# Optimization experiments

Hardware: AMD Instinct MI355X
Metric: run time of the kernel (lower is better)

## Reference

```python
import jax, jax.numpy as jnp
import numpy as np

HC = 4
C = 256
TMAX = 20
RMS_EPS = 1e-6
PRE_EPS = 0.0
SINKHORN_EPS = 1e-6
POST_MULT = 2.0


def setup_inputs() -> dict:
    key = jax.random.key(0)
    k1, k2, k3 = jax.random.split(key, 3)
    B, S = 8, 4096
    m = HC * HC + 2 * HC
    x = jax.random.normal(k1, (B, S, HC, C), dtype=jnp.float32)
    phi = jax.random.normal(k2, (HC * C, m), dtype=jnp.float32) * 0.02
    b = jnp.zeros((m,), dtype=jnp.float32)
    W = jax.random.normal(k3, (C, C), dtype=jnp.float32) * (1.0 / np.sqrt(C))
    return {
        "x": x, "phi": phi, "b": b,
        "alpha_pre": jnp.float32(1.0), "alpha_post": jnp.float32(1.0), "alpha_res": jnp.float32(1.0),
        "W": W,
    }


def _mhc_coeffs(x, phi, b, alpha_pre, alpha_post, alpha_res):
    # x: [..., HC, C] -> flatten streams, project, RMS-normalize logits.
    lead = x.shape[:-2]
    v = x.reshape(lead + (HC * C,))
    logits = jnp.einsum('...k,km->...m', v, phi)            # [..., m]
    rms = jnp.sqrt(jnp.mean(logits * logits, axis=-1, keepdims=True) + RMS_EPS)
    y = logits / rms + b                                     # [..., m]
    pre = y[..., :HC]
    post = y[..., HC:2 * HC]
    res = y[..., 2 * HC:].reshape(lead + (HC, HC))
    h_pre = jax.nn.sigmoid(alpha_pre * pre) + PRE_EPS        # [..., HC]
    h_post = POST_MULT * jax.nn.sigmoid(alpha_post * post)   # [..., HC]
    # Sinkhorn-Knopp: make exp(alpha_res * res) approximately doubly stochastic.
    P = jnp.exp(alpha_res * res)                             # [..., HC, HC]

    def step(P, _):
        P = P / (jnp.sum(P, axis=-1, keepdims=True) + SINKHORN_EPS)  # row norm
        P = P / (jnp.sum(P, axis=-2, keepdims=True) + SINKHORN_EPS)  # col norm
        return P, None

    P, _ = jax.lax.scan(step, P, None, length=TMAX)
    return h_pre, h_post, P


def reference(x, phi, b, alpha_pre, alpha_post, alpha_res, W):
    h_pre, h_post, h_res = _mhc_coeffs(x, phi, b, alpha_pre, alpha_post, alpha_res)
    # Pre-aggregate streams: x_in = sum_i h_pre[i] * x[i]
    x_in = jnp.einsum('...i,...ic->...c', h_pre, x)          # [..., C]
    # Wrapped layer: nn.Linear(C, C, bias=False) -> x_in @ W.T
    f_out = x_in @ W.T                                       # [..., C]
    # Post + residual: x_out[o] = sum_i h_res[o,i]*x[i] + h_post[o]*f_out
    x_out = jnp.einsum('...oi,...ic->...oc', h_res, x) + h_post[..., :, None] * f_out[..., None, :]
    return x_out
```

## Files before the change

### kernel.cpp

```cpp
#include <hip/hip_runtime.h>

typedef __attribute__((ext_vector_type(4))) float floatx4;
typedef __attribute__((ext_vector_type(8))) short short8;

__device__ __forceinline__ unsigned short f2bf(float f) {
    union { float f; unsigned int i; } v; v.f = f;
    unsigned int x = v.i;
    unsigned int r = (x + 0x7FFFu + ((x >> 16) & 1u)) >> 16;
    return (unsigned short)r;
}

__device__ __forceinline__ unsigned int cvtpk_bf16(float lo, float hi) {
    unsigned int r;
    asm("v_cvt_pk_bf16_f32 %0, %1, %2" : "=v"(r) : "v"(lo), "v"(hi));
    return r;
}

template<int CTRL>
__device__ __forceinline__ float dppf(float x) {
    return __int_as_float(__builtin_amdgcn_update_dpp(
        0, __float_as_int(x), CTRL, 0xF, 0xF, false));
}

__global__ void mhc_prep(const float* __restrict__ phi, const float* __restrict__ W,
                         unsigned short* __restrict__ phiF, unsigned short* __restrict__ WF) {
    int e = blockIdx.x * 256 + threadIdx.x;
    if (e < 32768) {
        int j = e & 7, lane = (e >> 3) & 63, nt = (e >> 9) & 1, ks = e >> 10;
        int n = nt * 16 + (lane & 15);
        int k = ks * 32 + ((lane >> 4) & 3) * 8 + j;
        float v = (n < 24) ? phi[k * 24 + n] : 0.0f;
        phiF[e] = f2bf(v);
    } else {
        int e2 = e - 32768;
        int j = e2 & 7, lane = (e2 >> 3) & 63, ks = (e2 >> 9) & 7, nt = e2 >> 12;
        int n = nt * 16 + (lane & 15);
        int k = ks * 32 + ((lane >> 4) & 3) * 8 + j;
        WF[e2] = f2bf(W[n * 256 + k]);
    }
}

#define TOK 8
#define XS_STRIDE 1032
#define XIN_STRIDE 264
#define CO_STRIDE 28
#define F_STRIDE 260

__global__ __launch_bounds__(256, 7) void mhc_main(
    const float* __restrict__ x, const float* __restrict__ bias,
    const float* __restrict__ s_ap, const float* __restrict__ s_apo,
    const float* __restrict__ s_ar,
    const unsigned short* __restrict__ phiF, const unsigned short* __restrict__ WF,
    float* __restrict__ out)
{
    __shared__ alignas(16) unsigned short xs[TOK * XS_STRIDE];
    __shared__ alignas(16) unsigned short xin[TOK * XIN_STRIDE];
    __shared__ alignas(16) float lgp[2][TOK * CO_STRIDE];
    __shared__ alignas(16) float coef[TOK * 24];
    float* fbuf = reinterpret_cast<float*>(xs);

    const int t = threadIdx.x;
    const int lane = t & 63;
    const int w = t >> 6;
    const int quad = lane >> 4;
    const int col = lane & 15;
    const long base = (long)blockIdx.x * (TOK * 1024);

    {
        const float4* xg = (const float4*)(x + base);
        #pragma unroll
        for (int ii = 0; ii < TOK; ++ii) {
            float4 v = xg[ii * 256 + t];
            uint2 pk;
            pk.x = cvtpk_bf16(v.x, v.y);
            pk.y = cvtpk_bf16(v.z, v.w);
            *reinterpret_cast<uint2*>(&xs[ii * XS_STRIDE + t * 4]) = pk;
        }
    }
    __syncthreads();

    {
        floatx4 acc = {0.0f, 0.0f, 0.0f, 0.0f};
        const int ntile = w & 1;
        const int kh = w >> 1;
        const int arow = col & 7;
        for (int ks = kh * 16; ks < kh * 16 + 16; ++ks) {
            short8 a = *reinterpret_cast<const short8*>(&xs[arow * XS_STRIDE + ks * 32 + quad * 8]);
            short8 b = *reinterpret_cast<const short8*>(&phiF[(ks * 2 + ntile) * 512 + lane * 8]);
            acc = __builtin_amdgcn_mfma_f32_16x16x32_bf16(a, b, acc, 0, 0, 0);
        }
        int n = ntile * 16 + col;
        if (n < 24 && quad < 2) {
            #pragma unroll
            for (int r = 0; r < 4; ++r)
                lgp[kh][(quad * 4 + r) * CO_STRIDE + n] = acc[r];
        }
    }
    __syncthreads();

    if (t < 128) {
        int g = t >> 4, p = t & 15;
        float a  = lgp[0][g * CO_STRIDE + p]      + lgp[1][g * CO_STRIDE + p];
        float b2 = (p < 8) ? (lgp[0][g * CO_STRIDE + 16 + p] + lgp[1][g * CO_STRIDE + 16 + p]) : 0.0f;
        float s = a * a + b2 * b2;
        s += dppf<0x121>(s);
        s += dppf<0x122>(s);
        s += dppf<0x124>(s);
        s += dppf<0x128>(s);
        float rinv = 1.0f / sqrtf(s * (1.0f / 24.0f) + 1e-6f);
        float lr = lgp[0][g * CO_STRIDE + 8 + p] + lgp[1][g * CO_STRIDE + 8 + p];
        float yP = lr * rinv + bias[8 + p];
        float P = expf(s_ar[0] * yP);
        for (int it = 0; it < 20; ++it) {
            float r = P + dppf<0x39>(P);
            r += dppf<0x4E>(r);
            P *= __builtin_amdgcn_rcpf(r + 1e-6f);
            float c = P + dppf<0x124>(P);
            c += dppf<0x128>(c);
            P *= __builtin_amdgcn_rcpf(c + 1e-6f);
        }
        coef[g * 24 + 8 + p] = P;
        if (p < 8) {
            float yh = a * rinv + bias[p];
            float h = (p < 4) ? 1.0f / (1.0f + expf(-s_ap[0] * yh))
                              : 2.0f / (1.0f + expf(-s_apo[0] * yh));
            coef[g * 24 + p] = h;
        }
    }
    __syncthreads();

    {
        const int cc = (t & 63) * 4;
        const int tok0 = w * 2;
        #pragma unroll
        for (int s = 0; s < 2; ++s) {
            int tok = tok0 + s;
            float4 h4 = *reinterpret_cast<const float4*>(&coef[tok * 24]);
            const float* xr = x + base + tok * 1024 + cc;
            float4 x0 = *reinterpret_cast<const float4*>(xr);
            float4 x1 = *reinterpret_cast<const float4*>(xr + 256);
            float4 x2 = *reinterpret_cast<const float4*>(xr + 512);
            float4 x3 = *reinterpret_cast<const float4*>(xr + 768);
            float4 sr;
            sr.x = h4.x * x0.x + h4.y * x1.x + h4.z * x2.x + h4.w * x3.x;
            sr.y = h4.x * x0.y + h4.y * x1.y + h4.z * x2.y + h4.w * x3.y;
            sr.z = h4.x * x0.z + h4.y * x1.z + h4.z * x2.z + h4.w * x3.z;
            sr.w = h4.x * x0.w + h4.y * x1.w + h4.z * x2.w + h4.w * x3.w;
            uint2 pk;
            pk.x = cvtpk_bf16(sr.x, sr.y);
            pk.y = cvtpk_bf16(sr.z, sr.w);
            *reinterpret_cast<uint2*>(&xin[tok * XIN_STRIDE + cc]) = pk;
        }
    }
    __syncthreads();

    {
        const int arow = col & 7;
        short8 afr[8];
        #pragma unroll
        for (int ks = 0; ks < 8; ++ks)
            afr[ks] = *reinterpret_cast<const short8*>(&xin[arow * XIN_STRIDE + ks * 32 + quad * 8]);
        floatx4 accs[4];
        #pragma unroll
        for (int nt = 0; nt < 4; ++nt) {
            floatx4 acc = {0.0f, 0.0f, 0.0f, 0.0f};
            int ntile = w * 4 + nt;
            #pragma unroll
            for (int ks = 0; ks < 8; ++ks) {
                short8 b = *reinterpret_cast<const short8*>(&WF[(ntile * 8 + ks) * 512 + lane * 8]);
                acc = __builtin_amdgcn_mfma_f32_16x16x32_bf16(afr[ks], b, acc, 0, 0, 0);
            }
            accs[nt] = acc;
        }
        if (quad < 2) {
            #pragma unroll
            for (int nt = 0; nt < 4; ++nt) {
                int n = (w * 4 + nt) * 16 + col;
                #pragma unroll
                for (int r = 0; r < 4; ++r)
                    fbuf[(quad * 4 + r) * F_STRIDE + n] = accs[nt][r];
            }
        }
    }
    __syncthreads();

    {
        const int cc = (t & 63) * 4;
        const int tok0 = w * 2;
        #pragma unroll
        for (int s = 0; s < 2; ++s) {
            int tok = tok0 + s;
            const float* cb = &coef[tok * 24];
            float4 hpo = *reinterpret_cast<const float4*>(cb + 4);
            float4 P0  = *reinterpret_cast<const float4*>(cb + 8);
            float4 P1  = *reinterpret_cast<const float4*>(cb + 12);
            float4 P2  = *reinterpret_cast<const float4*>(cb + 16);
            float4 P3  = *reinterpret_cast<const float4*>(cb + 20);
            const float* xr = x + base + tok * 1024 + cc;
            float4 x0 = *reinterpret_cast<const float4*>(xr);
            float4 x1 = *reinterpret_cast<const float4*>(xr + 256);
            float4 x2 = *reinterpret_cast<const float4*>(xr + 512);
            float4 x3 = *reinterpret_cast<const float4*>(xr + 768);
            float4 f  = *reinterpret_cast<const float4*>(&fbuf[tok * F_STRIDE + cc]);
            float* ob = out + base + tok * 1024 + cc;
            float4 o0, o1, o2, o3;
            o0.x = P0.x*x0.x + P0.y*x1.x + P0.z*x2.x + P0.w*x3.x + hpo.x*f.x;
            o0.y = P0.x*x0.y + P0.y*x1.y + P0.z*x2.y + P0.w*x3.y + hpo.x*f.y;
            o0.z = P0.x*x0.z + P0.y*x1.z + P0.z*x2.z + P0.w*x3.z + hpo.x*f.z;
            o0.w = P0.x*x0.w + P0.y*x1.w + P0.z*x2.w + P0.w*x3.w + hpo.x*f.w;
            o1.x = P1.x*x0.x + P1.y*x1.x + P1.z*x2.x + P1.w*x3.x + hpo.y*f.x;
            o1.y = P1.x*x0.y + P1.y*x1.y + P1.z*x2.y + P1.w*x3.y + hpo.y*f.y;
            o1.z = P1.x*x0.z + P1.y*x1.z + P1.z*x2.z + P1.w*x3.z + hpo.y*f.z;
            o1.w = P1.x*x0.w + P1.y*x1.w + P1.z*x2.w + P1.w*x3.w + hpo.y*f.w;
            o2.x = P2.x*x0.x + P2.y*x1.x + P2.z*x2.x + P2.w*x3.x + hpo.z*f.x;
            o2.y = P2.x*x0.y + P2.y*x1.y + P2.z*x2.y + P2.w*x3.y + hpo.z*f.y;
            o2.z = P2.x*x0.z + P2.y*x1.z + P2.z*x2.z + P2.w*x3.z + hpo.z*f.z;
            o2.w = P2.x*x0.w + P2.y*x1.w + P2.z*x2.w + P2.w*x3.w + hpo.z*f.w;
            o3.x = P3.x*x0.x + P3.y*x1.x + P3.z*x2.x + P3.w*x3.x + hpo.w*f.x;
            o3.y = P3.x*x0.y + P3.y*x1.y + P3.z*x2.y + P3.w*x3.y + hpo.w*f.y;
            o3.z = P3.x*x0.z + P3.y*x1.z + P3.z*x2.z + P3.w*x3.z + hpo.w*f.z;
            o3.w = P3.x*x0.w + P3.y*x1.w + P3.z*x2.w + P3.w*x3.w + hpo.w*f.w;
            *reinterpret_cast<float4*>(ob)       = o0;
            *reinterpret_cast<float4*>(ob + 256) = o1;
            *reinterpret_cast<float4*>(ob + 512) = o2;
            *reinterpret_cast<float4*>(ob + 768) = o3;
        }
    }
}

extern "C" void kernel_launch(void* const* d_in, const int* in_sizes, int n_in,
                              void* d_out, int out_size, void* d_ws, size_t ws_size,
                              hipStream_t stream) {
    const float* x    = (const float*)d_in[0];
    const float* phi  = (const float*)d_in[1];
    const float* bias = (const float*)d_in[2];
    const float* ap   = (const float*)d_in[3];
    const float* apo  = (const float*)d_in[4];
    const float* ar   = (const float*)d_in[5];
    const float* W    = (const float*)d_in[6];
    float* out = (float*)d_out;

    unsigned short* phiF = (unsigned short*)d_ws;
    unsigned short* WF   = (unsigned short*)d_ws + 32768;

    mhc_prep<<<384, 256, 0, stream>>>(phi, W, phiF, WF);
    mhc_main<<<4096, 256, 0, stream>>>(x, bias, ap, apo, ar, phiF, WF, out);
}
```

Baseline: 274.4 us.

## Reuse bf16 shared-memory x copy instead of re-reading fp32 x from global

The pre-aggregation and output stages now read x from the bf16 copy already staged in shared memory instead of reloading the fp32 input from global memory twice. The output is computed straight from the MFMA accumulators, which removes the fbuf staging pass and one barrier. The logits buffer is aliased onto the xin buffer to cut LDS use. The cost is that the residual term now uses bf16-rounded x, which lowers accuracy, and the output stores become scalar rather than float4, which may hurt write coalescing.

```diff
diff --git a/kernel.cpp b/kernel.cpp
--- a/kernel.cpp
+++ b/kernel.cpp
@@ -8,6 +8,10 @@
     unsigned int x = v.i;
     unsigned int r = (x + 0x7FFFu + ((x >> 16) & 1u)) >> 16;
     return (unsigned short)r;
+}
+__device__ __forceinline__ float bf2f(unsigned short u) {
+    union { unsigned int i; float f; } v; v.i = ((unsigned int)u) << 16;
+    return v.f;
 }
 
 __device__ __forceinline__ unsigned int cvtpk_bf16(float lo, float hi) {
@@ -44,7 +48,6 @@
 #define XS_STRIDE 1032
 #define XIN_STRIDE 264
 #define CO_STRIDE 28
-#define F_STRIDE 260
 
 __global__ __launch_bounds__(256, 7) void mhc_main(
     const float* __restrict__ x, const float* __restrict__ bias,
@@ -54,10 +57,9 @@
     float* __restrict__ out)
 {
     __shared__ alignas(16) unsigned short xs[TOK * XS_STRIDE];
-    __shared__ alignas(16) unsigned short xin[TOK * XIN_STRIDE];
-    __shared__ alignas(16) float lgp[2][TOK * CO_STRIDE];
+    __shared__ alignas(16) unsigned short xin_u[TOK * XIN_STRIDE];
     __shared__ alignas(16) float coef[TOK * 24];
-    float* fbuf = reinterpret_cast<float*>(xs);
+    float* lgp = reinterpret_cast<float*>(xin_u);
 
     const int t = threadIdx.x;
     const int lane = t & 63;
@@ -93,23 +95,24 @@
         if (n < 24 && quad < 2) {
             #pragma unroll
             for (int r = 0; r < 4; ++r)
-                lgp[kh][(quad * 4 + r) * CO_STRIDE + n] = acc[r];
+                lgp[kh * (TOK * CO_STRIDE) + (quad * 4 + r) * CO_STRIDE + n] = acc[r];
         }
     }
     __syncthreads();
 
     if (t < 128) {
         int g = t >> 4, p = t & 15;
-        float a  = lgp[0][g * CO_STRIDE + p]      + lgp[1][g * CO_STRIDE + p];
-        float b2 = (p < 8) ? (lgp[0][g * CO_STRIDE + 16 + p] + lgp[1][g * CO_STRIDE + 16 + p]) : 0.0f;
+        const float* l0 = lgp + g * CO_STRIDE;
+        const float* l1 = lgp + TOK * CO_STRIDE + g * CO_STRIDE;
+        float a  = l0[p] + l1[p];
+        float b2 = (p < 8) ? (l0[16 + p] + l1[16 + p]) : 0.0f;
         float s = a * a + b2 * b2;
         s += dppf<0x121>(s);
         s += dppf<0x122>(s);
         s += dppf<0x124>(s);
         s += dppf<0x128>(s);
         float rinv = 1.0f / sqrtf(s * (1.0f / 24.0f) + 1e-6f);
-        float lr = lgp[0][g * CO_STRIDE + 8 + p] + lgp[1][g * CO_STRIDE + 8 + p];
-        float yP = lr * rinv + bias[8 + p];
+        float yP = (l0[8 + p] + l1[8 + p]) * rinv + bias[8 + p];
         float P = expf(s_ar[0] * yP);
         for (int it = 0; it < 20; ++it) {
             float r = P + dppf<0x39>(P);
@@ -130,37 +133,25 @@
     __syncthreads();
 
     {
-        const int cc = (t & 63) * 4;
-        const int tok0 = w * 2;
-        #pragma unroll
-        for (int s = 0; s < 2; ++s) {
-            int tok = tok0 + s;
+        const int c = t;
+        #pragma unroll
+        for (int tok = 0; tok < TOK; ++tok) {
             float4 h4 = *reinterpret_cast<const float4*>(&coef[tok * 24]);
-            const float* xr = x + base + tok * 1024 + cc;
-            float4 x0 = *reinterpret_cast<const float4*>(xr);
-            float4 x1 = *reinterpret_cast<const float4*>(xr + 256);
-            float4 x2 = *reinterpret_cast<const float4*>(xr + 512);
-            float4 x3 = *reinterpret_cast<const float4*>(xr + 768);
-            float4 sr;
-            sr.x = h4.x * x0.x + h4.y * x1.x + h4.z * x2.x + h4.w * x3.x;
-            sr.y = h4.x * x0.y + h4.y * x1.y + h4.z * x2.y + h4.w * x3.y;
-            sr.z = h4.x * x0.z + h4.y * x1.z + h4.z * x2.z + h4.w * x3.z;
-            sr.w = h4.x * x0.w + h4.y * x1.w + h4.z * x2.w + h4.w * x3.w;
-            uint2 pk;
-            pk.x = cvtpk_bf16(sr.x, sr.y);
-            pk.y = cvtpk_bf16(sr.z, sr.w);
-            *reinterpret_cast<uint2*>(&xin[tok * XIN_STRIDE + cc]) = pk;
-        }
-    }
-    __syncthreads();
-
+            const unsigned short* xr = &xs[tok * XS_STRIDE + c];
+            float sv = h4.x * bf2f(xr[0]) + h4.y * bf2f(xr[256])
+                     + h4.z * bf2f(xr[512]) + h4.w * bf2f(xr[768]);
+            xin_u[tok * XIN_STRIDE + c] = f2bf(sv);
+        }
+    }
+    __syncthreads();
+
+    floatx4 accs[4];
     {
         const int arow = col & 7;
         short8 afr[8];
         #pragma unroll
         for (int ks = 0; ks < 8; ++ks)
-            afr[ks] = *reinterpret_cast<const short8*>(&xin[arow * XIN_STRIDE + ks * 32 + quad * 8]);
-        floatx4 accs[4];
+            afr[ks] = *reinterpret_cast<const short8*>(&xin_u[arow * XIN_STRIDE + ks * 32 + quad * 8]);
         #pragma unroll
         for (int nt = 0; nt < 4; ++nt) {
             floatx4 acc = {0.0f, 0.0f, 0.0f, 0.0f};
@@ -172,58 +163,28 @@
             }
             accs[nt] = acc;
         }
-        if (quad < 2) {
+    }
+
+    {
+        const int o0 = (quad >> 1) * 2;
+        #pragma unroll
+        for (int r = 0; r < 4; ++r) {
+            int tok = (quad & 1) * 4 + r;
+            const float* cb = &coef[tok * 24];
+            float hpoA = cb[4 + o0], hpoB = cb[5 + o0];
+            float4 PA = *reinterpret_cast<const float4*>(cb + 8 + 4 * o0);
+            float4 PB = *reinterpret_cast<const float4*>(cb + 12 + 4 * o0);
+            long ob = base + (long)tok * 1024 + (long)o0 * 256;
             #pragma unroll
             for (int nt = 0; nt < 4; ++nt) {
-                int n = (w * 4 + nt) * 16 + col;
-                #pragma unroll
-                for (int r = 0; r < 4; ++r)
-                    fbuf[(quad * 4 + r) * F_STRIDE + n] = accs[nt][r];
+                int c = (w * 4 + nt) * 16 + col;
+                float f = accs[nt][r];
+                const unsigned short* xr = &xs[tok * XS_STRIDE + c];
+                float x0 = bf2f(xr[0]),   x1 = bf2f(xr[256]);
+                float x2 = bf2f(xr[512]), x3 = bf2f(xr[768]);
+                out[ob + c]       = PA.x * x0 + PA.y * x1 + PA.z * x2 + PA.w * x3 + hpoA * f;
+                out[ob + 256 + c] = PB.x * x0 + PB.y * x1 + PB.z * x2 + PB.w * x3 + hpoB * f;
             }
-        }
-    }
-    __syncthreads();
-
-    {
-        const int cc = (t & 63) * 4;
-        const int tok0 = w * 2;
-        #pragma unroll
-        for (int s = 0; s < 2; ++s) {
-            int tok = tok0 + s;
-            const float* cb = &coef[tok * 24];
-            float4 hpo = *reinterpret_cast<const float4*>(cb + 4);
-            float4 P0  = *reinterpret_cast<const float4*>(cb + 8);
-            float4 P1  = *reinterpret_cast<const float4*>(cb + 12);
-            float4 P2  = *reinterpret_cast<const float4*>(cb + 16);
-            float4 P3  = *reinterpret_cast<const float4*>(cb + 20);
-            const float* xr = x + base + tok * 1024 + cc;
-            float4 x0 = *reinterpret_cast<const float4*>(xr);
-            float4 x1 = *reinterpret_cast<const float4*>(xr + 256);
-            float4 x2 = *reinterpret_cast<const float4*>(xr + 512);
-            float4 x3 = *reinterpret_cast<const float4*>(xr + 768);
-            float4 f  = *reinterpret_cast<const float4*>(&fbuf[tok * F_STRIDE + cc]);
-            float* ob = out + base + tok * 1024 + cc;
-            float4 o0, o1, o2, o3;
-            o0.x = P0.x*x0.x + P0.y*x1.x + P0.z*x2.x + P0.w*x3.x + hpo.x*f.x;
-            o0.y = P0.x*x0.y + P0.y*x1.y + P0.z*x2.y + P0.w*x3.y + hpo.x*f.y;
-            o0.z = P0.x*x0.z + P0.y*x1.z + P0.z*x2.z + P0.w*x3.z + hpo.x*f.z;
-            o0.w = P0.x*x0.w + P0.y*x1.w + P0.z*x2.w + P0.w*x3.w + hpo.x*f.w;
-            o1.x = P1.x*x0.x + P1.y*x1.x + P1.z*x2.x + P1.w*x3.x + hpo.y*f.x;
-            o1.y = P1.x*x0.y + P1.y*x1.y + P1.z*x2.y + P1.w*x3.y + hpo.y*f.y;
-            o1.z = P1.x*x0.z + P1.y*x1.z + P1.z*x2.z + P1.w*x3.z + hpo.y*f.z;
-            o1.w = P1.x*x0.w + P1.y*x1.w + P1.z*x2.w + P1.w*x3.w + hpo.y*f.w;
-            o2.x = P2.x*x0.x + P2.y*x1.x + P2.z*x2.x + P2.w*x3.x + hpo.z*f.x;
-            o2.y = P2.x*x0.y + P2.y*x1.y + P2.z*x2.y + P2.w*x3.y + hpo.z*f.y;
-            o2.z = P2.x*x0.z + P2.y*x1.z + P2.z*x2.z + P2.w*x3.z + hpo.z*f.z;
-            o2.w = P2.x*x0.w + P2.y*x1.w + P2.z*x2.w + P2.w*x3.w + hpo.z*f.w;
-            o3.x = P3.x*x0.x + P3.y*x1.x + P3.z*x2.x + P3.w*x3.x + hpo.w*f.x;
-            o3.y = P3.x*x0.y + P3.y*x1.y + P3.z*x2.y + P3.w*x3.y + hpo.w*f.y;
-            o3.z = P3.x*x0.z + P3.y*x1.z + P3.z*x2.z + P3.w*x3.z + hpo.w*f.z;
-            o3.w = P3.x*x0.w + P3.y*x1.w + P3.z*x2.w + P3.w*x3.w + hpo.w*f.w;
-            *reinterpret_cast<float4*>(ob)       = o0;
-            *reinterpret_cast<float4*>(ob + 256) = o1;
-            *reinterpret_cast<float4*>(ob + 512) = o2;
-            *reinterpret_cast<float4*>(ob + 768) = o3;
         }
     }
 }
```

New measurement: 262.1 us. 4.5% less time.
